# Kernel optimization log

Measured on AMD Instinct MI355X. Metric: run time of the kernel, lower is better.

Reference implementation:

```python
import jax, jax.numpy as jnp
import numpy as np

D_MODEL = 1024
N_HEAD = 16
D_HEAD = D_MODEL // N_HEAD


def setup_inputs() -> dict:
    key = jax.random.key(0)
    k1, k2, k3 = jax.random.split(key, 3)
    x = jax.random.normal(k1, (4, 1024, D_MODEL), dtype=jnp.float32)
    # torch Linear(d_model, 3*d_model, bias=False): weight [3*d_model, d_model], y = x @ W.T
    w_qkv = jax.random.normal(k2, (3 * D_MODEL, D_MODEL), dtype=jnp.float32) * (1.0 / np.sqrt(D_MODEL))
    w_out = jax.random.normal(k3, (D_MODEL, D_MODEL), dtype=jnp.float32) * (1.0 / np.sqrt(D_MODEL))
    return {"x": x, "w_qkv": w_qkv, "w_out": w_out}


def reference(x, w_qkv, w_out):
    B, T, C = x.shape
    qkv = x @ w_qkv.T                                   # [B,T,3C]
    qkv = qkv.reshape(B, T, 3, N_HEAD, D_HEAD)
    q = jnp.transpose(qkv[:, :, 0], (0, 2, 1, 3))       # [B,H,T,Dh]
    k = jnp.transpose(qkv[:, :, 1], (0, 2, 1, 3))
    v = jnp.transpose(qkv[:, :, 2], (0, 2, 1, 3))
    att = jnp.einsum('bhqd,bhkd->bhqk', q, k) / jnp.sqrt(jnp.float32(D_HEAD))
    causal = jnp.tril(jnp.ones((T, T), dtype=bool))
    att = jnp.where(causal[None, None], att, -jnp.inf)
    att = jax.nn.softmax(att, axis=-1)
    y = jnp.einsum('bhqk,bhkd->bhqd', att, v)           # [B,H,T,Dh]
    y = jnp.transpose(y, (0, 2, 1, 3)).reshape(B, T, C)
    return y @ w_out.T
```

## Files before the change

### kernel.cpp

```cpp
#include <hip/hip_runtime.h>
#include <hip/hip_bf16.h>
#include <stdint.h>

#define DM 1024
#define NH 16
#define DH 64
#define BB 4
#define TT 1024
#define MR (BB*TT)

typedef __attribute__((ext_vector_type(8))) short bf16x8;
typedef __attribute__((ext_vector_type(4))) float f32x4;

typedef unsigned int __attribute__((address_space(1))) uint_g;
typedef unsigned int __attribute__((address_space(3))) uint_l;

static __device__ __forceinline__ void gload_lds16(const void* g, void* l) {
  __builtin_amdgcn_global_load_lds((const uint_g*)g, (uint_l*)l, 16, 0, 0);
}

static __device__ __forceinline__ void fence() { asm volatile("" ::: "memory"); }

static __device__ __forceinline__ unsigned short f2bf(float f) {
  union { float f; unsigned int u; } v; v.f = f;
  unsigned int r = v.u + 0x7fffu + ((v.u >> 16) & 1u);
  return (unsigned short)(r >> 16);
}
static __device__ __forceinline__ unsigned short f2bf_fast(float f) {
  union { float f; unsigned int u; } v; v.f = f;
  return (unsigned short)((v.u + 0x8000u) >> 16);
}

__global__ __launch_bounds__(256) void k_cvt3(const float* __restrict__ x,
    const float* __restrict__ w1, const float* __restrict__ w2,
    unsigned short* __restrict__ xb, unsigned short* __restrict__ wqb,
    unsigned short* __restrict__ wob) {
  const int n1 = (MR * DM) / 4, n2 = (3 * DM * DM) / 4, n3 = (DM * DM) / 4;
  const int total = n1 + n2 + n3;
  for (int u = blockIdx.x * 256 + threadIdx.x; u < total; u += gridDim.x * 256) {
    const float* src; unsigned short* dst; int i;
    if (u < n1)           { src = x;  dst = xb;  i = u; }
    else if (u < n1 + n2) { src = w1; dst = wqb; i = u - n1; }
    else                  { src = w2; dst = wob; i = u - n1 - n2; }
    float4 v = reinterpret_cast<const float4*>(src)[i];
    ushort4 o;
    o.x = f2bf(v.x); o.y = f2bf(v.y); o.z = f2bf(v.z); o.w = f2bf(v.w);
    reinterpret_cast<ushort4*>(dst)[i] = o;
  }
}

template<int EPI>
__global__ __launch_bounds__(256) void k_gemm(
    const unsigned short* __restrict__ A, const unsigned short* __restrict__ Bw,
    float* __restrict__ Of, unsigned short* __restrict__ qb,
    unsigned short* __restrict__ kb, unsigned short* __restrict__ vtb,
    int N, int K, int tiles_n) {
  __shared__ unsigned short At[3][128 * 32];
  __shared__ unsigned short Bt[3][128 * 32];
  int tid = threadIdx.x;
  int w = tid >> 6, l = tid & 63;
  int l15 = l & 15, k8 = l >> 4;
  int nwg = gridDim.x;
  int cpx = nwg >> 3;
  int wg = blockIdx.x;
  int swz = (wg & 7) * cpx + (wg >> 3);
  int tm = swz / tiles_n, tn = swz % tiles_n;
  int m0 = tm << 7, n0 = tn << 7;

  f32x4 acc[4][4];
  #pragma unroll
  for (int i = 0; i < 4; ++i)
    #pragma unroll
    for (int j = 0; j < 4; ++j) acc[i][j] = (f32x4){0.f, 0.f, 0.f, 0.f};

  int srow = (w << 4) + (l >> 2);
  int sch = l & 3;
  int mrb = ((w >> 1) << 6) + l15;
  int nrb = ((w & 1) << 6) + l15;

  auto stage = [&](int buf, int kk) {
    #pragma unroll
    for (int p = 0; p < 2; ++p) {
      int row = srow + (p << 6);
      int c = sch ^ ((row >> 1) & 3);
      int seg = w + (p << 2);
      gload_lds16(A + (size_t)(m0 + row) * K + kk + (c << 3), &At[buf][seg << 9]);
      gload_lds16(Bw + (size_t)(n0 + row) * K + kk + (c << 3), &Bt[buf][seg << 9]);
    }
  };

  const int nt = K >> 5;
  stage(0, 0);
  stage(1, 32);
  asm volatile("s_waitcnt vmcnt(4)" ::: "memory");
  fence(); __builtin_amdgcn_s_barrier(); fence();

  int rd = 0;
  for (int t = 0; t < nt; ++t) {
    int st = (rd == 0) ? 2 : rd - 1;
    if (t + 2 < nt) stage(st, (t + 2) << 5);
    bf16x8 a[4], b[4];
    #pragma unroll
    for (int mf = 0; mf < 4; ++mf) {
      int row = mrb + (mf << 4);
      a[mf] = *(const bf16x8*)&At[rd][(row << 5) + ((k8 ^ ((row >> 1) & 3)) << 3)];
    }
    #pragma unroll
    for (int nf = 0; nf < 4; ++nf) {
      int row = nrb + (nf << 4);
      b[nf] = *(const bf16x8*)&Bt[rd][(row << 5) + ((k8 ^ ((row >> 1) & 3)) << 3)];
    }
    #pragma unroll
    for (int mf = 0; mf < 4; ++mf)
      #pragma unroll
      for (int nf = 0; nf < 4; ++nf)
        acc[mf][nf] = __builtin_amdgcn_mfma_f32_16x16x32_bf16(a[mf], b[nf], acc[mf][nf], 0, 0, 0);
    if (t + 2 < nt)      { asm volatile("s_waitcnt vmcnt(4)" ::: "memory"); }
    else if (t + 1 < nt) { asm volatile("s_waitcnt vmcnt(0)" ::: "memory"); }
    fence(); __builtin_amdgcn_s_barrier(); fence();
    rd = (rd == 2) ? 0 : rd + 1;
  }

  #pragma unroll
  for (int mf = 0; mf < 4; ++mf) {
    #pragma unroll
    for (int nf = 0; nf < 4; ++nf) {
      int n = n0 + ((w & 1) << 6) + (nf << 4) + l15;
      int m_base = m0 + ((w >> 1) << 6) + (mf << 4) + (k8 << 2);
      if (EPI == 1) {
        #pragma unroll
        for (int r = 0; r < 4; ++r)
          Of[(size_t)(m_base + r) * N + n] = acc[mf][nf][r];
      } else {
        int s = n >> 10, rem = n & 1023;
        int h = rem >> 6, d = rem & 63;
        #pragma unroll
        for (int r = 0; r < 4; ++r) {
          int m = m_base + r;
          int bb = m >> 10, t = m & 1023;
          float v = acc[mf][nf][r];
          if (s == 0)
            qb[((size_t)(bb * NH + h) * TT + t) * DH + d] = f2bf(v * 0.125f);
          else if (s == 1)
            kb[((size_t)(bb * NH + h) * TT + t) * DH + d] = f2bf(v);
          else
            vtb[((size_t)(bb * NH + h) * DH + d) * TT + t] = f2bf(v);
        }
      }
    }
  }
}

__global__ __launch_bounds__(512) void k_attn(
    const unsigned short* __restrict__ qb, const unsigned short* __restrict__ kb,
    const unsigned short* __restrict__ vtb, unsigned short* __restrict__ yb) {
  __shared__ unsigned short Kt[3][64 * 64];
  __shared__ unsigned short Vt[3][64 * 64];
  __shared__ unsigned short Pl[8][16][72];
  int tid = threadIdx.x, w = tid >> 6, l = tid & 63;
  int l15 = l & 15, k8 = l >> 4;
  int bh = blockIdx.x >> 3;
  int qt = blockIdx.x & 7;
  int q0 = qt << 7;
  const unsigned short* Kb = kb + (size_t)bh * TT * DH;
  const unsigned short* Vb = vtb + (size_t)bh * DH * TT;
  const unsigned short* Qb = qb + (size_t)bh * TT * DH;

  int qrow = q0 + (w << 4) + l15;
  bf16x8 qf[2];
  #pragma unroll
  for (int c = 0; c < 2; ++c)
    qf[c] = *(const bf16x8*)&Qb[(size_t)qrow * DH + (c << 5) + (k8 << 3)];

  f32x4 y[4];
  #pragma unroll
  for (int i = 0; i < 4; ++i) y[i] = (f32x4){0.f, 0.f, 0.f, 0.f};
  float mrow = -INFINITY, lrow = 0.f;

  int srow = l >> 3;
  int sch = l & 7;

  auto stage = [&](int buf, int j0) {
    int row = (w << 3) + srow;
    int c = sch ^ (row & 7);
    gload_lds16(Kb + (size_t)(j0 + row) * DH + (c << 3), &Kt[buf][(w << 3) << 6]);
    gload_lds16(Vb + (size_t)row * TT + j0 + (c << 3), &Vt[buf][(w << 3) << 6]);
  };

  const int ns = (q0 >> 6) + 2;
  stage(0, 0);
  stage(1, 64);
  asm volatile("s_waitcnt vmcnt(2)" ::: "memory");
  fence(); __builtin_amdgcn_s_barrier(); fence();

  int rd = 0;
  for (int t = 0; t < ns; ++t) {
    int j0 = t << 6;
    int st = (rd == 0) ? 2 : rd - 1;
    if (t + 2 < ns) stage(st, (t + 2) << 6);

    f32x4 s[4];
    #pragma unroll
    for (int f = 0; f < 4; ++f) s[f] = (f32x4){0.f, 0.f, 0.f, 0.f};
    __builtin_amdgcn_s_setprio(1);
    #pragma unroll
    for (int c = 0; c < 2; ++c) {
      #pragma unroll
      for (int f = 0; f < 4; ++f) {
        int row = (f << 4) + l15;
        bf16x8 ak = *(const bf16x8*)&Kt[rd][(row << 6) + ((((c << 2) + k8) ^ (row & 7)) << 3)];
        s[f] = __builtin_amdgcn_mfma_f32_16x16x32_bf16(ak, qf[c], s[f], 0, 0, 0);
      }
    }
    __builtin_amdgcn_s_setprio(0);

    if (j0 + 64 > q0 + (w << 4)) {
      #pragma unroll
      for (int f = 0; f < 4; ++f)
        #pragma unroll
        for (int r = 0; r < 4; ++r)
          if (j0 + (f << 4) + (k8 << 2) + r > qrow) s[f][r] = -INFINITY;
    }

    float pmax = -INFINITY;
    #pragma unroll
    for (int f = 0; f < 4; ++f)
      #pragma unroll
      for (int r = 0; r < 4; ++r) pmax = fmaxf(pmax, s[f][r]);
    pmax = fmaxf(pmax, __shfl_xor(pmax, 16, 64));
    pmax = fmaxf(pmax, __shfl_xor(pmax, 32, 64));

    bool skip = __all(pmax - mrow <= 8.0f);
    float mnew = skip ? mrow : fmaxf(mrow, pmax);
    float psum = 0.f;
    #pragma unroll
    for (int f = 0; f < 4; ++f)
      #pragma unroll
      for (int r = 0; r < 4; ++r) {
        float p = __expf(s[f][r] - mnew);
        s[f][r] = p;
        psum += p;
      }
    psum += __shfl_xor(psum, 16, 64);
    psum += __shfl_xor(psum, 32, 64);
    if (!skip) {
      float alpha = __expf(mrow - mnew);
      lrow *= alpha;
      #pragma unroll
      for (int mf = 0; mf < 4; ++mf) y[mf] *= alpha;
      mrow = mnew;
    }
    lrow += psum;

    #pragma unroll
    for (int f = 0; f < 4; ++f) {
      ushort4 pk;
      pk.x = f2bf_fast(s[f][0]); pk.y = f2bf_fast(s[f][1]);
      pk.z = f2bf_fast(s[f][2]); pk.w = f2bf_fast(s[f][3]);
      *(ushort4*)&Pl[w][l15][(f << 4) + (k8 << 2)] = pk;
    }
    asm volatile("s_waitcnt lgkmcnt(0)" ::: "memory");
    __builtin_amdgcn_sched_barrier(0);

    __builtin_amdgcn_s_setprio(1);
    #pragma unroll
    for (int c = 0; c < 2; ++c) {
      bf16x8 bp = *(const bf16x8*)&Pl[w][l15][(c << 5) + (k8 << 3)];
      #pragma unroll
      for (int mf = 0; mf < 4; ++mf) {
        int dr = (mf << 4) + l15;
        bf16x8 av = *(const bf16x8*)&Vt[rd][(dr << 6) + ((((c << 2) + k8) ^ (dr & 7)) << 3)];
        y[mf] = __builtin_amdgcn_mfma_f32_16x16x32_bf16(av, bp, y[mf], 0, 0, 0);
      }
    }
    __builtin_amdgcn_s_setprio(0);

    if (t + 2 < ns)      { asm volatile("s_waitcnt vmcnt(2)" ::: "memory"); }
    else if (t + 1 < ns) { asm volatile("s_waitcnt vmcnt(0)" ::: "memory"); }
    fence(); __builtin_amdgcn_s_barrier(); fence();
    rd = (rd == 2) ? 0 : rd + 1;
  }

  float inv = 1.f / lrow;
  int bb = bh >> 4, h = bh & 15;
  #pragma unroll
  for (int mf = 0; mf < 4; ++mf) {
    ushort4 o;
    o.x = f2bf(y[mf][0] * inv);
    o.y = f2bf(y[mf][1] * inv);
    o.z = f2bf(y[mf][2] * inv);
    o.w = f2bf(y[mf][3] * inv);
    *(ushort4*)&yb[((size_t)(bb * TT + qrow) << 10) + (h << 6) + (mf << 4) + (k8 << 2)] = o;
  }
}

extern "C" void kernel_launch(void* const* d_in, const int* in_sizes, int n_in,
                              void* d_out, int out_size, void* d_ws, size_t ws_size,
                              hipStream_t stream) {
  const float* x    = (const float*)d_in[0];
  const float* wqkv = (const float*)d_in[1];
  const float* wout = (const float*)d_in[2];
  char* ws = (char*)d_ws;
  unsigned short* xb  = (unsigned short*)(ws + (size_t)0);
  unsigned short* wqb = (unsigned short*)(ws + ((size_t)8  << 20));
  unsigned short* wob = (unsigned short*)(ws + ((size_t)14 << 20));
  unsigned short* qbv = (unsigned short*)(ws + ((size_t)16 << 20));
  unsigned short* kbv = (unsigned short*)(ws + ((size_t)24 << 20));
  unsigned short* vtb = (unsigned short*)(ws + ((size_t)32 << 20));
  unsigned short* yb  = (unsigned short*)(ws + ((size_t)40 << 20));

  k_cvt3<<<2048, 256, 0, stream>>>(x, wqkv, wout, xb, wqb, wob);
  k_gemm<0><<<768, 256, 0, stream>>>(xb, wqb, nullptr, qbv, kbv, vtb, 3 * DM, DM, 24);
  k_attn<<<512, 512, 0, stream>>>(qbv, kbv, vtb, yb);
  k_gemm<1><<<256, 256, 0, stream>>>(yb, wob, (float*)d_out, nullptr, nullptr, nullptr, DM, DM, 8);
}
```

Measured before the change: 112.6 us.

## Load GEMM A operand directly to registers and double-buffer attention K/V

The GEMM stops staging the A tile through LDS. Each wave now loads its A fragments straight from global memory into registers, one k-step ahead, while B stays on the triple-buffered LDS path, and the main loop is unrolled by two to ping-pong the register buffers. The attention kernel drops from triple to double buffering of K/V, with a full vmcnt(0) wait each step. This lowers LDS use and LDS traffic but adds redundant global A loads across waves and exposes more load latency in attention.

Result: slower. 142.1 us (+26.3%).

```diff
diff --git a/kernel.cpp b/kernel.cpp
--- a/kernel.cpp
+++ b/kernel.cpp
@@ -54,8 +54,8 @@
     const unsigned short* __restrict__ A, const unsigned short* __restrict__ Bw,
     float* __restrict__ Of, unsigned short* __restrict__ qb,
     unsigned short* __restrict__ kb, unsigned short* __restrict__ vtb,
-    int N, int K, int tiles_n) {
-  __shared__ unsigned short At[3][128 * 32];
+    int N, int tiles_n) {
+  const int K = DM;
   __shared__ unsigned short Bt[3][128 * 32];
   int tid = threadIdx.x;
   int w = tid >> 6, l = tid & 63;
@@ -75,36 +75,37 @@
 
   int srow = (w << 4) + (l >> 2);
   int sch = l & 3;
-  int mrb = ((w >> 1) << 6) + l15;
   int nrb = ((w & 1) << 6) + l15;
 
-  auto stage = [&](int buf, int kk) {
+  auto stageB = [&](int buf, int t) {
     #pragma unroll
     for (int p = 0; p < 2; ++p) {
       int row = srow + (p << 6);
       int c = sch ^ ((row >> 1) & 3);
       int seg = w + (p << 2);
-      gload_lds16(A + (size_t)(m0 + row) * K + kk + (c << 3), &At[buf][seg << 9]);
-      gload_lds16(Bw + (size_t)(n0 + row) * K + kk + (c << 3), &Bt[buf][seg << 9]);
+      gload_lds16(Bw + (size_t)(n0 + row) * K + (t << 5) + (c << 3), &Bt[buf][seg << 9]);
     }
   };
+  auto loadA = [&](bf16x8 (&dst)[4], int kk) {
+    #pragma unroll
+    for (int mf = 0; mf < 4; ++mf) {
+      int row = m0 + ((w >> 1) << 6) + (mf << 4) + l15;
+      dst[mf] = *(const bf16x8*)&A[(size_t)row * K + kk + (k8 << 3)];
+    }
+  };
 
   const int nt = K >> 5;
-  stage(0, 0);
-  stage(1, 32);
-  asm volatile("s_waitcnt vmcnt(4)" ::: "memory");
+  bf16x8 a0[4], a1[4];
+  loadA(a0, 0);
+  stageB(0, 0);
+  stageB(1, 1);
+  asm volatile("s_waitcnt vmcnt(2)" ::: "memory");
   fence(); __builtin_amdgcn_s_barrier(); fence();
 
-  int rd = 0;
-  for (int t = 0; t < nt; ++t) {
-    int st = (rd == 0) ? 2 : rd - 1;
-    if (t + 2 < nt) stage(st, (t + 2) << 5);
-    bf16x8 a[4], b[4];
-    #pragma unroll
-    for (int mf = 0; mf < 4; ++mf) {
-      int row = mrb + (mf << 4);
-      a[mf] = *(const bf16x8*)&At[rd][(row << 5) + ((k8 ^ ((row >> 1) & 3)) << 3)];
-    }
+  auto iter = [&](int t, bf16x8 (&acur)[4], bf16x8 (&anxt)[4], int rd, int st) {
+    if (t + 1 < nt) loadA(anxt, (t + 1) << 5);
+    if (t + 2 < nt) stageB(st, t + 2);
+    bf16x8 b[4];
     #pragma unroll
     for (int nf = 0; nf < 4; ++nf) {
       int row = nrb + (nf << 4);
@@ -114,11 +115,20 @@
     for (int mf = 0; mf < 4; ++mf)
       #pragma unroll
       for (int nf = 0; nf < 4; ++nf)
-        acc[mf][nf] = __builtin_amdgcn_mfma_f32_16x16x32_bf16(a[mf], b[nf], acc[mf][nf], 0, 0, 0);
-    if (t + 2 < nt)      { asm volatile("s_waitcnt vmcnt(4)" ::: "memory"); }
+        acc[mf][nf] = __builtin_amdgcn_mfma_f32_16x16x32_bf16(acur[mf], b[nf], acc[mf][nf], 0, 0, 0);
+    if (t + 2 < nt)      { asm volatile("s_waitcnt vmcnt(2)" ::: "memory"); }
     else if (t + 1 < nt) { asm volatile("s_waitcnt vmcnt(0)" ::: "memory"); }
     fence(); __builtin_amdgcn_s_barrier(); fence();
-    rd = (rd == 2) ? 0 : rd + 1;
+  };
+
+  int rd = 0;
+  for (int t = 0; t < nt; t += 2) {
+    int st0 = (rd == 0) ? 2 : rd - 1;
+    iter(t, a0, a1, rd, st0);
+    int rd1 = (rd == 2) ? 0 : rd + 1;
+    int st1 = (rd1 == 0) ? 2 : rd1 - 1;
+    iter(t + 1, a1, a0, rd1, st1);
+    rd = (rd1 == 2) ? 0 : rd1 + 1;
   }
 
   #pragma unroll
@@ -154,8 +164,8 @@
 __global__ __launch_bounds__(512) void k_attn(
     const unsigned short* __restrict__ qb, const unsigned short* __restrict__ kb,
     const unsigned short* __restrict__ vtb, unsigned short* __restrict__ yb) {
-  __shared__ unsigned short Kt[3][64 * 64];
-  __shared__ unsigned short Vt[3][64 * 64];
+  __shared__ unsigned short Kt[2][64 * 64];
+  __shared__ unsigned short Vt[2][64 * 64];
   __shared__ unsigned short Pl[8][16][72];
   int tid = threadIdx.x, w = tid >> 6, l = tid & 63;
   int l15 = l & 15, k8 = l >> 4;
@@ -189,15 +199,13 @@
 
   const int ns = (q0 >> 6) + 2;
   stage(0, 0);
-  stage(1, 64);
-  asm volatile("s_waitcnt vmcnt(2)" ::: "memory");
+  asm volatile("s_waitcnt vmcnt(0)" ::: "memory");
   fence(); __builtin_amdgcn_s_barrier(); fence();
 
-  int rd = 0;
+  int cur = 0;
   for (int t = 0; t < ns; ++t) {
     int j0 = t << 6;
-    int st = (rd == 0) ? 2 : rd - 1;
-    if (t + 2 < ns) stage(st, (t + 2) << 6);
+    if (t + 1 < ns) stage(cur ^ 1, (t + 1) << 6);
 
     f32x4 s[4];
     #pragma unroll
@@ -208,7 +216,7 @@
       #pragma unroll
       for (int f = 0; f < 4; ++f) {
         int row = (f << 4) + l15;
-        bf16x8 ak = *(const bf16x8*)&Kt[rd][(row << 6) + ((((c << 2) + k8) ^ (row & 7)) << 3)];
+        bf16x8 ak = *(const bf16x8*)&Kt[cur][(row << 6) + ((((c << 2) + k8) ^ (row & 7)) << 3)];
         s[f] = __builtin_amdgcn_mfma_f32_16x16x32_bf16(ak, qf[c], s[f], 0, 0, 0);
       }
     }
@@ -269,16 +277,15 @@
       #pragma unroll
       for (int mf = 0; mf < 4; ++mf) {
         int dr = (mf << 4) + l15;
-        bf16x8 av = *(const bf16x8*)&Vt[rd][(dr << 6) + ((((c << 2) + k8) ^ (dr & 7)) << 3)];
+        bf16x8 av = *(const bf16x8*)&Vt[cur][(dr << 6) + ((((c << 2) + k8) ^ (dr & 7)) << 3)];
         y[mf] = __builtin_amdgcn_mfma_f32_16x16x32_bf16(av, bp, y[mf], 0, 0, 0);
       }
     }
     __builtin_amdgcn_s_setprio(0);
 
-    if (t + 2 < ns)      { asm volatile("s_waitcnt vmcnt(2)" ::: "memory"); }
-    else if (t + 1 < ns) { asm volatile("s_waitcnt vmcnt(0)" ::: "memory"); }
+    asm volatile("s_waitcnt vmcnt(0)" ::: "memory");
     fence(); __builtin_amdgcn_s_barrier(); fence();
-    rd = (rd == 2) ? 0 : rd + 1;
+    cur ^= 1;
   }
 
   float inv = 1.f / lrow;
@@ -310,7 +317,7 @@
   unsigned short* yb  = (unsigned short*)(ws + ((size_t)40 << 20));
 
   k_cvt3<<<2048, 256, 0, stream>>>(x, wqkv, wout, xb, wqb, wob);
-  k_gemm<0><<<768, 256, 0, stream>>>(xb, wqb, nullptr, qbv, kbv, vtb, 3 * DM, DM, 24);
+  k_gemm<0><<<768, 256, 0, stream>>>(xb, wqb, nullptr, qbv, kbv, vtb, 3 * DM, 24);
   k_attn<<<512, 512, 0, stream>>>(qbv, kbv, vtb, yb);
-  k_gemm<1><<<256, 256, 0, stream>>>(yb, wob, (float*)d_out, nullptr, nullptr, nullptr, DM, DM, 8);
-}
+  k_gemm<1><<<256, 256, 0, stream>>>(yb, wob, (float*)d_out, nullptr, nullptr, nullptr, DM, 8);
+}
```

## Widen QKV GEMM tile to 128x256 and double-buffer attention K/V

Applied to the files above, without the earlier changes.

The QKV projection GEMM becomes a dedicated kernel with a 128x256 output tile per workgroup (8 N-fragments per wave), which halves the grid to 384 blocks and raises operand reuse per LDS load. The output GEMM is specialised with constant sizes. The attention kernel drops from triple to double buffering of K/V tiles with a full vmcnt(0) wait each iteration, which cuts LDS use but exposes more load latency. The larger accumulator tile raises register pressure, and the smaller grid may lower occupancy or tail balance.

New measurement: 125.4 us. 1.11x slower.

```diff
diff --git a/kernel.cpp b/kernel.cpp
--- a/kernel.cpp
+++ b/kernel.cpp
@@ -49,21 +49,115 @@
   }
 }
 
-template<int EPI>
-__global__ __launch_bounds__(256) void k_gemm(
+__global__ __launch_bounds__(256, 2) void k_gemm0(
     const unsigned short* __restrict__ A, const unsigned short* __restrict__ Bw,
-    float* __restrict__ Of, unsigned short* __restrict__ qb,
-    unsigned short* __restrict__ kb, unsigned short* __restrict__ vtb,
-    int N, int K, int tiles_n) {
+    unsigned short* __restrict__ qb, unsigned short* __restrict__ kb,
+    unsigned short* __restrict__ vtb) {
+  const int K = DM;
+  __shared__ unsigned short At[3][128 * 32];
+  __shared__ unsigned short Bt[3][256 * 32];
+  int tid = threadIdx.x;
+  int w = tid >> 6, l = tid & 63;
+  int l15 = l & 15, k8 = l >> 4;
+  int wm = w >> 1, wn = w & 1;
+  int wg = blockIdx.x;
+  int swz = (wg & 7) * 48 + (wg >> 3);
+  int tm = swz / 12, tn = swz % 12;
+  int m0 = tm << 7, n0 = tn << 8;
+
+  f32x4 acc[4][8];
+  #pragma unroll
+  for (int i = 0; i < 4; ++i)
+    #pragma unroll
+    for (int j = 0; j < 8; ++j) acc[i][j] = (f32x4){0.f, 0.f, 0.f, 0.f};
+
+  int srl = l >> 2;
+  int sch = l & 3;
+
+  auto stage = [&](int buf, int t) {
+    #pragma unroll
+    for (int q = 0; q < 2; ++q) {
+      int seg = (w << 1) + q;
+      int row = (seg << 4) + srl;
+      int c = sch ^ ((row >> 1) & 3);
+      gload_lds16(A + (size_t)(m0 + row) * K + (t << 5) + (c << 3), &At[buf][seg << 9]);
+    }
+    #pragma unroll
+    for (int q = 0; q < 4; ++q) {
+      int seg = (w << 2) + q;
+      int row = (seg << 4) + srl;
+      int c = sch ^ ((row >> 1) & 3);
+      gload_lds16(Bw + (size_t)(n0 + row) * K + (t << 5) + (c << 3), &Bt[buf][seg << 9]);
+    }
+  };
+
+  const int nt = K >> 5;
+  stage(0, 0);
+  stage(1, 1);
+  asm volatile("s_waitcnt vmcnt(6)" ::: "memory");
+  fence(); __builtin_amdgcn_s_barrier(); fence();
+
+  int rd = 0;
+  for (int t = 0; t < nt; ++t) {
+    int st = (rd == 0) ? 2 : rd - 1;
+    if (t + 2 < nt) stage(st, t + 2);
+    bf16x8 a[4], b[8];
+    #pragma unroll
+    for (int mf = 0; mf < 4; ++mf) {
+      int row = (wm << 6) + (mf << 4) + l15;
+      a[mf] = *(const bf16x8*)&At[rd][(row << 5) + ((k8 ^ ((row >> 1) & 3)) << 3)];
+    }
+    #pragma unroll
+    for (int nf = 0; nf < 8; ++nf) {
+      int row = (wn << 7) + (nf << 4) + l15;
+      b[nf] = *(const bf16x8*)&Bt[rd][(row << 5) + ((k8 ^ ((row >> 1) & 3)) << 3)];
+    }
+    #pragma unroll
+    for (int mf = 0; mf < 4; ++mf)
+      #pragma unroll
+      for (int nf = 0; nf < 8; ++nf)
+        acc[mf][nf] = __builtin_amdgcn_mfma_f32_16x16x32_bf16(a[mf], b[nf], acc[mf][nf], 0, 0, 0);
+    if (t + 2 < nt)      { asm volatile("s_waitcnt vmcnt(6)" ::: "memory"); }
+    else if (t + 1 < nt) { asm volatile("s_waitcnt vmcnt(0)" ::: "memory"); }
+    fence(); __builtin_amdgcn_s_barrier(); fence();
+    rd = (rd == 2) ? 0 : rd + 1;
+  }
+
+  #pragma unroll
+  for (int mf = 0; mf < 4; ++mf) {
+    #pragma unroll
+    for (int nf = 0; nf < 8; ++nf) {
+      int n = n0 + (wn << 7) + (nf << 4) + l15;
+      int m_base = m0 + (wm << 6) + (mf << 4) + (k8 << 2);
+      int s = n >> 10, rem = n & 1023;
+      int h = rem >> 6, d = rem & 63;
+      #pragma unroll
+      for (int r = 0; r < 4; ++r) {
+        int m = m_base + r;
+        int bb = m >> 10, t = m & 1023;
+        float v = acc[mf][nf][r];
+        if (s == 0)
+          qb[((size_t)(bb * NH + h) * TT + t) * DH + d] = f2bf(v * 0.125f);
+        else if (s == 1)
+          kb[((size_t)(bb * NH + h) * TT + t) * DH + d] = f2bf(v);
+        else
+          vtb[((size_t)(bb * NH + h) * DH + d) * TT + t] = f2bf(v);
+      }
+    }
+  }
+}
+
+__global__ __launch_bounds__(256) void k_gemm1(
+    const unsigned short* __restrict__ A, const unsigned short* __restrict__ Bw,
+    float* __restrict__ Of) {
+  const int N = DM, K = DM, tiles_n = 8;
   __shared__ unsigned short At[3][128 * 32];
   __shared__ unsigned short Bt[3][128 * 32];
   int tid = threadIdx.x;
   int w = tid >> 6, l = tid & 63;
   int l15 = l & 15, k8 = l >> 4;
-  int nwg = gridDim.x;
-  int cpx = nwg >> 3;
   int wg = blockIdx.x;
-  int swz = (wg & 7) * cpx + (wg >> 3);
+  int swz = (wg & 7) * 32 + (wg >> 3);
   int tm = swz / tiles_n, tn = swz % tiles_n;
   int m0 = tm << 7, n0 = tn << 7;
 
@@ -122,40 +216,22 @@
   }
 
   #pragma unroll
-  for (int mf = 0; mf < 4; ++mf) {
+  for (int mf = 0; mf < 4; ++mf)
     #pragma unroll
     for (int nf = 0; nf < 4; ++nf) {
       int n = n0 + ((w & 1) << 6) + (nf << 4) + l15;
       int m_base = m0 + ((w >> 1) << 6) + (mf << 4) + (k8 << 2);
-      if (EPI == 1) {
-        #pragma unroll
-        for (int r = 0; r < 4; ++r)
-          Of[(size_t)(m_base + r) * N + n] = acc[mf][nf][r];
-      } else {
-        int s = n >> 10, rem = n & 1023;
-        int h = rem >> 6, d = rem & 63;
-        #pragma unroll
-        for (int r = 0; r < 4; ++r) {
-          int m = m_base + r;
-          int bb = m >> 10, t = m & 1023;
-          float v = acc[mf][nf][r];
-          if (s == 0)
-            qb[((size_t)(bb * NH + h) * TT + t) * DH + d] = f2bf(v * 0.125f);
-          else if (s == 1)
-            kb[((size_t)(bb * NH + h) * TT + t) * DH + d] = f2bf(v);
-          else
-            vtb[((size_t)(bb * NH + h) * DH + d) * TT + t] = f2bf(v);
-        }
-      }
-    }
-  }
+      #pragma unroll
+      for (int r = 0; r < 4; ++r)
+        Of[(size_t)(m_base + r) * N + n] = acc[mf][nf][r];
+    }
 }
 
 __global__ __launch_bounds__(512) void k_attn(
     const unsigned short* __restrict__ qb, const unsigned short* __restrict__ kb,
     const unsigned short* __restrict__ vtb, unsigned short* __restrict__ yb) {
-  __shared__ unsigned short Kt[3][64 * 64];
-  __shared__ unsigned short Vt[3][64 * 64];
+  __shared__ unsigned short Kt[2][64 * 64];
+  __shared__ unsigned short Vt[2][64 * 64];
   __shared__ unsigned short Pl[8][16][72];
   int tid = threadIdx.x, w = tid >> 6, l = tid & 63;
   int l15 = l & 15, k8 = l >> 4;
@@ -189,15 +265,13 @@
 
   const int ns = (q0 >> 6) + 2;
   stage(0, 0);
-  stage(1, 64);
-  asm volatile("s_waitcnt vmcnt(2)" ::: "memory");
+  asm volatile("s_waitcnt vmcnt(0)" ::: "memory");
   fence(); __builtin_amdgcn_s_barrier(); fence();
 
-  int rd = 0;
+  int cur = 0;
   for (int t = 0; t < ns; ++t) {
     int j0 = t << 6;
-    int st = (rd == 0) ? 2 : rd - 1;
-    if (t + 2 < ns) stage(st, (t + 2) << 6);
+    if (t + 1 < ns) stage(cur ^ 1, (t + 1) << 6);
 
     f32x4 s[4];
     #pragma unroll
@@ -208,7 +282,7 @@
       #pragma unroll
       for (int f = 0; f < 4; ++f) {
         int row = (f << 4) + l15;
-        bf16x8 ak = *(const bf16x8*)&Kt[rd][(row << 6) + ((((c << 2) + k8) ^ (row & 7)) << 3)];
+        bf16x8 ak = *(const bf16x8*)&Kt[cur][(row << 6) + ((((c << 2) + k8) ^ (row & 7)) << 3)];
         s[f] = __builtin_amdgcn_mfma_f32_16x16x32_bf16(ak, qf[c], s[f], 0, 0, 0);
       }
     }
@@ -269,16 +343,15 @@
       #pragma unroll
       for (int mf = 0; mf < 4; ++mf) {
         int dr = (mf << 4) + l15;
-        bf16x8 av = *(const bf16x8*)&Vt[rd][(dr << 6) + ((((c << 2) + k8) ^ (dr & 7)) << 3)];
+        bf16x8 av = *(const bf16x8*)&Vt[cur][(dr << 6) + ((((c << 2) + k8) ^ (dr & 7)) << 3)];
         y[mf] = __builtin_amdgcn_mfma_f32_16x16x32_bf16(av, bp, y[mf], 0, 0, 0);
       }
     }
     __builtin_amdgcn_s_setprio(0);
 
-    if (t + 2 < ns)      { asm volatile("s_waitcnt vmcnt(2)" ::: "memory"); }
-    else if (t + 1 < ns) { asm volatile("s_waitcnt vmcnt(0)" ::: "memory"); }
+    asm volatile("s_waitcnt vmcnt(0)" ::: "memory");
     fence(); __builtin_amdgcn_s_barrier(); fence();
-    rd = (rd == 2) ? 0 : rd + 1;
+    cur ^= 1;
   }
 
   float inv = 1.f / lrow;
@@ -310,7 +383,7 @@
   unsigned short* yb  = (unsigned short*)(ws + ((size_t)40 << 20));
 
   k_cvt3<<<2048, 256, 0, stream>>>(x, wqkv, wout, xb, wqb, wob);
-  k_gemm<0><<<768, 256, 0, stream>>>(xb, wqb, nullptr, qbv, kbv, vtb, 3 * DM, DM, 24);
+  k_gemm0<<<384, 256, 0, stream>>>(xb, wqb, qbv, kbv, vtb);
   k_attn<<<512, 512, 0, stream>>>(qbv, kbv, vtb, yb);
-  k_gemm<1><<<256, 256, 0, stream>>>(yb, wob, (float*)d_out, nullptr, nullptr, nullptr, DM, DM, 8);
-}
+  k_gemm1<<<256, 256, 0, stream>>>(yb, wob, (float*)d_out);
+}
```
